# Optimization experiments

Hardware: AMD Instinct MI355X
Metric: run time of the kernel (lower is better)

The kernel has to match this reference:

```python
import jax, jax.numpy as jnp
import numpy as np

N_LAYERS = 6
N_HEADS = 16
HIDDEN = 1024
HEAD = HIDDEN // N_HEADS  # 64
FFWD = 4096
VOCAB = 32000
WIN = 512
EMBED = 128
BATCH = 4
NEG_INF = -1.0e9


def layer_norm(x, bias, scale, eps=1e-6):
    m = jnp.mean(x, axis=-1, keepdims=True)
    v = jnp.mean(jnp.square(x - m), axis=-1, keepdims=True)
    return (x - m) * jax.lax.rsqrt(v + eps) * scale + bias


def setup_inputs() -> dict:
    key = jax.random.key(0)
    ks = jax.random.split(key, 16)

    def rn(k, shape):
        return 0.1 * jax.random.normal(k, shape, jnp.float32)

    return {
        "x_input": jax.random.randint(ks[0], (BATCH, WIN), 0, VOCAB),
        "prev_inputs": jax.random.normal(ks[1], (N_LAYERS, BATCH, WIN, HIDDEN), jnp.float32),
        "W_emb_dec": rn(ks[2], (VOCAB, EMBED)),
        "W_dec_lin": rn(ks[3], (EMBED, HIDDEN)),
        "p_decoder": rn(ks[4], (HIDDEN, VOCAB)),
        "p_d_q": rn(ks[5], (N_LAYERS, HIDDEN, HIDDEN)),
        "p_d_k": rn(ks[6], (N_LAYERS, HIDDEN, HIDDEN)),
        "p_d_v": rn(ks[7], (N_LAYERS, HIDDEN, HIDDEN)),
        "p_d_c": rn(ks[8], (N_LAYERS, HIDDEN, HIDDEN)),
        "p_d_ff1": rn(ks[9], (N_LAYERS, HIDDEN, FFWD)),
        "p_d_ff2": rn(ks[10], (N_LAYERS, FFWD, HIDDEN)),
        "b_d_ff1": jnp.zeros((N_LAYERS, FFWD), jnp.float32),
        "b_d_ff2": jnp.zeros((N_LAYERS, HIDDEN), jnp.float32),
        "b_d_bias_1": jnp.zeros((N_LAYERS, HIDDEN), jnp.float32),
        "b_d_bias_2": jnp.zeros((N_LAYERS, HIDDEN), jnp.float32),
        "b_d_scale_1": jnp.ones((N_LAYERS, HIDDEN), jnp.float32),
        "b_d_scale_2": jnp.ones((N_LAYERS, HIDDEN), jnp.float32),
        "x_emb_pos_dec": rn(ks[11], (N_LAYERS, 2 * WIN, HIDDEN)),
    }


def reference(x_input, prev_inputs, W_emb_dec, W_dec_lin, p_decoder,
              p_d_q, p_d_k, p_d_v, p_d_c, p_d_ff1, p_d_ff2,
              b_d_ff1, b_d_ff2, b_d_bias_1, b_d_bias_2,
              b_d_scale_1, b_d_scale_2, x_emb_pos_dec):
    L = x_input.shape[1]
    # token embedding (scaled by 1/sqrt(hidden)) then linear to hidden
    tok = W_emb_dec[x_input] * (HIDDEN ** -0.5)        # [B, L, E]
    h0 = jnp.einsum('ble,eh->blh', tok, W_dec_lin)     # [B, L, H]

    mask_len = L + WIN
    mask = NEG_INF * (1.0 - jnp.tril(jnp.ones((mask_len, mask_len), jnp.float32)))

    def split_heads(x):
        b, t, _ = x.shape
        return x.reshape(b, t, N_HEADS, HEAD).transpose(0, 2, 1, 3)  # [B, nH, T, d]

    def layer_fn(layer_input, p):
        Wq, Wk, Wv, Wc, Wf1, Wf2, bf1, bf2, b1, s1, b2, s2, pos, prev = p
        # concat cached window with current input, add positional embedding
        x = pos[None] + jnp.concatenate([prev, layer_input], axis=1)  # [B, 2W, H]
        q = split_heads(x @ Wq) * (HEAD ** -0.5)
        k = split_heads(x @ Wk)
        v = split_heads(x @ Wv)
        scores = jnp.einsum('bhqd,bhkd->bhqk', q, k) + mask
        alphas = jax.nn.softmax(scores, axis=-1)
        o = jnp.einsum('bhqk,bhkd->bhqd', alphas, v)
        o = o.transpose(0, 2, 1, 3).reshape(x.shape)  # combine heads
        attn = o @ Wc
        # var_type == 'norm_add': residual + LN(sublayer)
        x_self = x + layer_norm(attn, b1, s1)
        ff = jnp.maximum(x_self @ Wf1 + bf1, 0.0) @ Wf2 + bf2
        y = x_self + layer_norm(ff, b2, s2)
        new = y[:, WIN:, :]  # drop the cached-window positions
        return new, new

    params = (p_d_q, p_d_k, p_d_v, p_d_c, p_d_ff1, p_d_ff2,
              b_d_ff1, b_d_ff2, b_d_bias_1, b_d_scale_1,
              b_d_bias_2, b_d_scale_2, x_emb_pos_dec, prev_inputs)
    _, dec_outputs = jax.lax.scan(layer_fn, h0, params)  # [n_layers, B, L, H]
    dec_logits = jnp.einsum('blh,hv->blv', dec_outputs[-1], p_decoder)
    return (dec_logits, dec_outputs)
```

## Files before the change

### kernel.cpp

```cpp
#include <hip/hip_runtime.h>
#include <hip/hip_bf16.h>

#define NL   6
#define NH   16
#define HID  1024
#define HD   64
#define FFW  4096
#define VOC  32000
#define WINN 512
#define EMB  128
#define NB   4
#define TT   1024

typedef __attribute__((ext_vector_type(8))) _Float16 f16x8;
typedef __attribute__((ext_vector_type(8))) short    b16x8;
typedef __attribute__((ext_vector_type(4))) float    f32x4;

__device__ __forceinline__ ushort f2b(float f) {
    __hip_bfloat16 h = __float2bfloat16(f);
    return *reinterpret_cast<ushort*>(&h);
}
__device__ __forceinline__ void split16(float f, ushort& hb, ushort& lb) {
    _Float16 h = (_Float16)f;
    _Float16 l = (_Float16)((f - (float)h) * 2048.0f);
    hb = __builtin_bit_cast(ushort, h);
    lb = __builtin_bit_cast(ushort, l);
}

__global__ __launch_bounds__(256) void embed_kernel(
    const int* __restrict__ xin, const float* __restrict__ Wemb,
    const float* __restrict__ Wlin, float* __restrict__ h0)
{
    int row = blockIdx.x;
    int tok = xin[row];
    __shared__ float tk[EMB];
    if (threadIdx.x < EMB) tk[threadIdx.x] = Wemb[tok * EMB + threadIdx.x] * 0.03125f;
    __syncthreads();
    for (int j = 0; j < 4; ++j) {
        int c = threadIdx.x + 256 * j;
        float acc = 0.f;
        for (int e = 0; e < EMB; ++e) acc += tk[e] * Wlin[e * HID + c];
        h0[(long)row * HID + c] = acc;
    }
}

__global__ __launch_bounds__(256) void build_x_kernel(
    const float* __restrict__ pos, const float* __restrict__ prev,
    const float* __restrict__ cur, float* __restrict__ x,
    ushort* __restrict__ xh, ushort* __restrict__ xl)
{
    int i4 = blockIdx.x * blockDim.x + threadIdx.x;
    if (i4 >= NB * TT * HID / 4) return;
    int h4 = i4 % (HID / 4);
    int bt = i4 / (HID / 4);
    int t = bt % TT, b = bt / TT;
    float4 p = ((const float4*)pos)[t * (HID / 4) + h4];
    float4 s;
    if (t < WINN) s = ((const float4*)prev)[(long)(b * WINN + t) * (HID / 4) + h4];
    else          s = ((const float4*)cur)[(long)(b * WINN + (t - WINN)) * (HID / 4) + h4];
    float4 r; r.x = p.x + s.x; r.y = p.y + s.y; r.z = p.z + s.z; r.w = p.w + s.w;
    ((float4*)x)[i4] = r;
    ushort4 uh, ul;
    split16(r.x, uh.x, ul.x); split16(r.y, uh.y, ul.y);
    split16(r.z, uh.z, ul.z); split16(r.w, uh.w, ul.w);
    ((ushort4*)xh)[i4] = uh;
    ((ushort4*)xl)[i4] = ul;
}

__global__ __launch_bounds__(256) void wsplit_kernel(
    const float* __restrict__ W, ushort* __restrict__ Wth, ushort* __restrict__ Wtl,
    int K, int N)
{
    __shared__ float ts[32][33];
    int n0 = blockIdx.x * 32, k0 = blockIdx.y * 32;
    int tr = threadIdx.x >> 5, tc = threadIdx.x & 31;
#pragma unroll
    for (int j = 0; j < 4; ++j)
        ts[tr + j * 8][tc] = W[(long)(k0 + tr + j * 8) * N + n0 + tc];
    __syncthreads();
#pragma unroll
    for (int j = 0; j < 4; ++j) {
        int n = tr + j * 8;
        ushort hb, lb;
        split16(ts[tc][n], hb, lb);
        long idx = (long)(n0 + n) * K + k0 + tc;
        Wth[idx] = hb;
        Wtl[idx] = lb;
    }
}

__global__ __launch_bounds__(256) void vtrans_kernel(
    const ushort* __restrict__ vh, const ushort* __restrict__ vl,
    ushort* __restrict__ vth, ushort* __restrict__ vtl, int src_stride)
{
    __shared__ ushort th[32][33], tl[32][33];
    int n0 = blockIdx.x * 32, r0 = blockIdx.y * 32;
    int tr = threadIdx.x >> 5, tc = threadIdx.x & 31;
#pragma unroll
    for (int j = 0; j < 4; ++j) {
        long g = (long)(r0 + tr + j * 8) * src_stride + n0 + tc;
        th[tr + j * 8][tc] = vh[g];
        tl[tr + j * 8][tc] = vl[g];
    }
    __syncthreads();
#pragma unroll
    for (int j = 0; j < 4; ++j) {
        long g = (long)(n0 + tr + j * 8) * (NB * TT) + r0 + tc;
        vth[g] = th[tc][tr + j * 8];
        vtl[g] = tl[tc][tr + j * 8];
    }
}

__global__ __launch_bounds__(256) void hgemm(
    const ushort* __restrict__ Ah, const ushort* __restrict__ Al,
    const ushort* __restrict__ Bh, const ushort* __restrict__ Bl,
    float* __restrict__ Cf0, float* __restrict__ Cf1,
    int M, int N, int K_stride, int Ksub,
    float scale, const float* __restrict__ bias, int relu, int amap)
{
    __shared__ ushort Ash[128 * 40];
    __shared__ ushort Asl[128 * 40];
    __shared__ ushort Bsh[64 * 40];
    __shared__ ushort Bsl[64 * 40];
    const int tid  = threadIdx.x;
    const int rb   = blockIdx.y * 128;
    const int cb   = blockIdx.x * 64;
    const int z    = blockIdx.z;
    const int k_off = z * Ksub;
    float* __restrict__ Cf = z ? Cf1 : Cf0;
    const float* bias_eff = (z == 0) ? bias : nullptr;
    const int wave = tid >> 6, lane = tid & 63;
    const int wr   = (wave >> 1) * 64;
    const int wc   = (wave & 1) * 32;
    const int lr   = lane & 15;
    const int kh   = lane >> 4;

    const int sar = tid >> 1;
    const int sak = (tid & 1) * 16;
    int gra = rb + sar;
    long marow = amap ? (long)((gra >> 9) * 1024 + 512 + (gra & 511)) : (long)gra;
    const ushort* pAh = Ah + marow * K_stride + k_off + sak;
    const ushort* pAl = Al + marow * K_stride + k_off + sak;
    const int wA0 = sar * 40 + sak, wA1 = wA0 + 8;
    const int sbr = tid >> 2;
    const int sbk = (tid & 3) * 8;
    const ushort* pBh = Bh + (long)(cb + sbr) * K_stride + k_off + sbk;
    const ushort* pBl = Bl + (long)(cb + sbr) * K_stride + k_off + sbk;
    const int wB0 = sbr * 40 + sbk;

    int aoff[4], boff[2];
#pragma unroll
    for (int m = 0; m < 4; ++m) aoff[m] = (wr + m * 16 + lr) * 40 + kh * 8;
#pragma unroll
    for (int n = 0; n < 2; ++n) boff[n] = (wc + n * 16 + lr) * 40 + kh * 8;

    f32x4 accH[4][2], accL[4][2];
#pragma unroll
    for (int m = 0; m < 4; ++m)
#pragma unroll
        for (int n = 0; n < 2; ++n) {
            accH[m][n] = (f32x4){0.f, 0.f, 0.f, 0.f};
            accL[m][n] = (f32x4){0.f, 0.f, 0.f, 0.f};
        }

    for (int k0 = 0; k0 < Ksub; k0 += 32) {
        uint4 ah0 = *(const uint4*)(pAh + k0);
        uint4 ah1 = *(const uint4*)(pAh + k0 + 8);
        uint4 al0 = *(const uint4*)(pAl + k0);
        uint4 al1 = *(const uint4*)(pAl + k0 + 8);
        uint4 bh0 = *(const uint4*)(pBh + k0);
        uint4 bl0 = *(const uint4*)(pBl + k0);
        __syncthreads();
        *(uint4*)(Ash + wA0) = ah0; *(uint4*)(Ash + wA1) = ah1;
        *(uint4*)(Asl + wA0) = al0; *(uint4*)(Asl + wA1) = al1;
        *(uint4*)(Bsh + wB0) = bh0;
        *(uint4*)(Bsl + wB0) = bl0;
        __syncthreads();
        f16x8 afh[4], afl[4], bfh[2], bfl[2];
#pragma unroll
        for (int m = 0; m < 4; ++m) {
            afh[m] = *(const f16x8*)(Ash + aoff[m]);
            afl[m] = *(const f16x8*)(Asl + aoff[m]);
        }
#pragma unroll
        for (int n = 0; n < 2; ++n) {
            bfh[n] = *(const f16x8*)(Bsh + boff[n]);
            bfl[n] = *(const f16x8*)(Bsl + boff[n]);
        }
#pragma unroll
        for (int m = 0; m < 4; ++m)
#pragma unroll
            for (int n = 0; n < 2; ++n) {
                accH[m][n] = __builtin_amdgcn_mfma_f32_16x16x32_f16(afh[m], bfh[n], accH[m][n], 0, 0, 0);
                accL[m][n] = __builtin_amdgcn_mfma_f32_16x16x32_f16(afh[m], bfl[n], accL[m][n], 0, 0, 0);
                accL[m][n] = __builtin_amdgcn_mfma_f32_16x16x32_f16(afl[m], bfh[n], accL[m][n], 0, 0, 0);
            }
    }

#pragma unroll
    for (int m = 0; m < 4; ++m) {
        int row0 = rb + wr + m * 16 + kh * 4;
#pragma unroll
        for (int n = 0; n < 2; ++n) {
            int col = cb + wc + n * 16 + lr;
            float bv = bias_eff ? bias_eff[col] : 0.f;
#pragma unroll
            for (int r = 0; r < 4; ++r) {
                float v = (accH[m][n][r] + accL[m][n][r] * (1.f / 2048.f)) * scale + bv;
                if (relu) v = fmaxf(v, 0.f);
                Cf[(long)(row0 + r) * N + col] = v;
            }
        }
    }
}

__global__ __launch_bounds__(512) void hgemm8(
    const ushort* __restrict__ Ah, const ushort* __restrict__ Al,
    const ushort* __restrict__ Bh, const ushort* __restrict__ Bl,
    ushort* __restrict__ Chh, ushort* __restrict__ Cll,
    int M, int N, int K_stride,
    float scale, const float* __restrict__ bias, int relu)
{
    __shared__ ushort Ash[128 * 40];
    __shared__ ushort Asl[128 * 40];
    __shared__ ushort Bsh[128 * 40];
    __shared__ ushort Bsl[128 * 40];
    const int tid  = threadIdx.x;
    const int rb   = blockIdx.y * 128;
    const int cb   = blockIdx.x * 128;
    const int wave = tid >> 6, lane = tid & 63;
    const int wr   = (wave >> 2) * 64;
    const int wc   = (wave & 3) * 32;
    const int lr   = lane & 15;
    const int kh   = lane >> 4;

    const int srow = tid >> 2;
    const int sk   = (tid & 3) * 8;
    const ushort* pAh = Ah + (long)(rb + srow) * K_stride + sk;
    const ushort* pAl = Al + (long)(rb + srow) * K_stride + sk;
    const ushort* pBh = Bh + (long)(cb + srow) * K_stride + sk;
    const ushort* pBl = Bl + (long)(cb + srow) * K_stride + sk;
    const int woff = srow * 40 + sk;

    int aoff[4], boff[2];
#pragma unroll
    for (int m = 0; m < 4; ++m) aoff[m] = (wr + m * 16 + lr) * 40 + kh * 8;
#pragma unroll
    for (int n = 0; n < 2; ++n) boff[n] = (wc + n * 16 + lr) * 40 + kh * 8;

    f32x4 accH[4][2], accL[4][2];
#pragma unroll
    for (int m = 0; m < 4; ++m)
#pragma unroll
        for (int n = 0; n < 2; ++n) {
            accH[m][n] = (f32x4){0.f, 0.f, 0.f, 0.f};
            accL[m][n] = (f32x4){0.f, 0.f, 0.f, 0.f};
        }

    for (int k0 = 0; k0 < K_stride; k0 += 32) {
        uint4 ah = *(const uint4*)(pAh + k0);
        uint4 al = *(const uint4*)(pAl + k0);
        uint4 bh = *(const uint4*)(pBh + k0);
        uint4 bl = *(const uint4*)(pBl + k0);
        __syncthreads();
        *(uint4*)(Ash + woff) = ah;
        *(uint4*)(Asl + woff) = al;
        *(uint4*)(Bsh + woff) = bh;
        *(uint4*)(Bsl + woff) = bl;
        __syncthreads();
        f16x8 afh[4], afl[4], bfh[2], bfl[2];
#pragma unroll
        for (int m = 0; m < 4; ++m) {
            afh[m] = *(const f16x8*)(Ash + aoff[m]);
            afl[m] = *(const f16x8*)(Asl + aoff[m]);
        }
#pragma unroll
        for (int n = 0; n < 2; ++n) {
            bfh[n] = *(const f16x8*)(Bsh + boff[n]);
            bfl[n] = *(const f16x8*)(Bsl + boff[n]);
        }
#pragma unroll
        for (int m = 0; m < 4; ++m)
#pragma unroll
            for (int n = 0; n < 2; ++n) {
                accH[m][n] = __builtin_amdgcn_mfma_f32_16x16x32_f16(afh[m], bfh[n], accH[m][n], 0, 0, 0);
                accL[m][n] = __builtin_amdgcn_mfma_f32_16x16x32_f16(afh[m], bfl[n], accL[m][n], 0, 0, 0);
                accL[m][n] = __builtin_amdgcn_mfma_f32_16x16x32_f16(afl[m], bfh[n], accL[m][n], 0, 0, 0);
            }
    }

#pragma unroll
    for (int m = 0; m < 4; ++m) {
        int row0 = rb + wr + m * 16 + kh * 4;
#pragma unroll
        for (int n = 0; n < 2; ++n) {
            int col = cb + wc + n * 16 + lr;
            float bv = bias ? bias[col] : 0.f;
#pragma unroll
            for (int r = 0; r < 4; ++r) {
                float v = (accH[m][n][r] + accL[m][n][r] * (1.f / 2048.f)) * scale + bv;
                if (relu) v = fmaxf(v, 0.f);
                long idx = (long)(row0 + r) * N + col;
                ushort hb, lb; split16(v, hb, lb);
                Chh[idx] = hb; Cll[idx] = lb;
            }
        }
    }
}

__global__ __launch_bounds__(256) void fattn_mfma(
    const float* __restrict__ qa, const float* __restrict__ qb,
    const ushort* __restrict__ kbh, const ushort* __restrict__ kbl, int kstr,
    const ushort* __restrict__ vth, const ushort* __restrict__ vtl,
    ushort* __restrict__ oh, ushort* __restrict__ ol)
{
    __shared__ __align__(16) ushort ksh[64 * 72];
    __shared__ __align__(16) ushort ksl[64 * 72];
    __shared__ __align__(16) ushort vsh[64 * 72];
    __shared__ __align__(16) ushort vsl[64 * 72];
    const int qt = blockIdx.x, h = blockIdx.y, b = blockIdx.z;
    const int tid = threadIdx.x;
    const int wave = tid >> 6, lane = tid & 63;
    const int lr = lane & 15, kg4 = lane >> 4;
    const int qbase = b * WINN + qt * 64;

    f16x8 qfh[2], qfl[2];
#pragma unroll
    for (int c = 0; c < 2; ++c) {
        long ga = (long)(qbase + wave * 16 + lr) * HID + h * HD + c * 32 + kg4 * 8;
        float4 a0 = *(const float4*)(qa + ga);
        float4 a1 = *(const float4*)(qa + ga + 4);
        float4 b0 = *(const float4*)(qb + ga);
        float4 b1 = *(const float4*)(qb + ga + 4);
        float qv[8] = {a0.x + b0.x, a0.y + b0.y, a0.z + b0.z, a0.w + b0.w,
                       a1.x + b1.x, a1.y + b1.y, a1.z + b1.z, a1.w + b1.w};
        ushort uh[8], ul[8];
#pragma unroll
        for (int j = 0; j < 8; ++j) split16(qv[j], uh[j], ul[j]);
        qfh[c] = *(const f16x8*)uh;
        qfl[c] = *(const f16x8*)ul;
    }

    f32x4 accOH[4], accOL[4];
#pragma unroll
    for (int d = 0; d < 4; ++d) {
        accOH[d] = (f32x4){0.f, 0.f, 0.f, 0.f};
        accOL[d] = (f32x4){0.f, 0.f, 0.f, 0.f};
    }
    float mrow[4], lrow[4];
#pragma unroll
    for (int r = 0; r < 4; ++r) { mrow[r] = -3.0e38f; lrow[r] = 0.f; }

    const int sr = tid >> 2;
    const int sd = (tid & 3) * 16;

    const int ktmax = 9 + qt;
    for (int kt = 0; kt < ktmax; ++kt) {
        __syncthreads();
        {
            long gk = (long)(b * TT + kt * 64 + sr) * kstr + h * HD + sd;
            uint4 h0 = *(const uint4*)(kbh + gk);
            uint4 h1 = *(const uint4*)(kbh + gk + 8);
            uint4 l0 = *(const uint4*)(kbl + gk);
            uint4 l1 = *(const uint4*)(kbl + gk + 8);
            long gv = (long)(h * HD + sr) * (NB * TT) + b * TT + kt * 64 + sd;
            uint4 vh0 = *(const uint4*)(vth + gv);
            uint4 vh1 = *(const uint4*)(vth + gv + 8);
            uint4 vl0 = *(const uint4*)(vtl + gv);
            uint4 vl1 = *(const uint4*)(vtl + gv + 8);
            *(uint4*)(ksh + sr * 72 + sd) = h0;
            *(uint4*)(ksh + sr * 72 + sd + 8) = h1;
            *(uint4*)(ksl + sr * 72 + sd) = l0;
            *(uint4*)(ksl + sr * 72 + sd + 8) = l1;
            *(uint4*)(vsh + sr * 72 + sd) = vh0;
            *(uint4*)(vsh + sr * 72 + sd + 8) = vh1;
            *(uint4*)(vsl + sr * 72 + sd) = vl0;
            *(uint4*)(vsl + sr * 72 + sd + 8) = vl1;
        }
        __syncthreads();

        f32x4 sH[4], sL[4];
#pragma unroll
        for (int n = 0; n < 4; ++n) {
            sH[n] = (f32x4){0.f, 0.f, 0.f, 0.f};
            sL[n] = (f32x4){0.f, 0.f, 0.f, 0.f};
        }
#pragma unroll
        for (int c = 0; c < 2; ++c) {
#pragma unroll
            for (int n = 0; n < 4; ++n) {
                int ad = (n * 16 + lr) * 72 + c * 32 + kg4 * 8;
                f16x8 bh = *(const f16x8*)(ksh + ad);
                f16x8 bl = *(const f16x8*)(ksl + ad);
                sH[n] = __builtin_amdgcn_mfma_f32_16x16x32_f16(qfh[c], bh, sH[n], 0, 0, 0);
                sL[n] = __builtin_amdgcn_mfma_f32_16x16x32_f16(qfh[c], bl, sL[n], 0, 0, 0);
                sL[n] = __builtin_amdgcn_mfma_f32_16x16x32_f16(qfl[c], bh, sL[n], 0, 0, 0);
            }
        }
        float S[4][4];
#pragma unroll
        for (int n = 0; n < 4; ++n)
#pragma unroll
            for (int r = 0; r < 4; ++r)
                S[n][r] = sH[n][r] + sL[n][r] * (1.f / 2048.f);

        if (kt == ktmax - 1) {
#pragma unroll
            for (int r = 0; r < 4; ++r) {
                int qi = WINN + qt * 64 + wave * 16 + kg4 * 4 + r;
#pragma unroll
                for (int n = 0; n < 4; ++n) {
                    int kg = kt * 64 + n * 16 + lr;
                    if (kg > qi) S[n][r] = -1e9f;
                }
            }
        }

#pragma unroll
        for (int r = 0; r < 4; ++r) {
            float mx = fmaxf(fmaxf(S[0][r], S[1][r]), fmaxf(S[2][r], S[3][r]));
            mx = fmaxf(mx, __shfl_xor(mx, 1));
            mx = fmaxf(mx, __shfl_xor(mx, 2));
            mx = fmaxf(mx, __shfl_xor(mx, 4));
            mx = fmaxf(mx, __shfl_xor(mx, 8));
            float mnew = fmaxf(mrow[r], mx);
            float alpha = __expf(mrow[r] - mnew);
            float rs = 0.f;
#pragma unroll
            for (int n = 0; n < 4; ++n) { S[n][r] = __expf(S[n][r] - mnew); rs += S[n][r]; }
            rs += __shfl_xor(rs, 1);
            rs += __shfl_xor(rs, 2);
            rs += __shfl_xor(rs, 4);
            rs += __shfl_xor(rs, 8);
            lrow[r] = lrow[r] * alpha + rs;
            mrow[r] = mnew;
#pragma unroll
            for (int d = 0; d < 4; ++d) { accOH[d][r] *= alpha; accOL[d][r] *= alpha; }
        }

        __syncthreads();
#pragma unroll
        for (int n = 0; n < 4; ++n)
#pragma unroll
            for (int r = 0; r < 4; ++r) {
                ushort hb, lb;
                split16(S[n][r], hb, lb);
                int ad = (wave * 16 + kg4 * 4 + r) * 72 + n * 16 + lr;
                ksh[ad] = hb;
                ksl[ad] = lb;
            }
        f16x8 pfh[2], pfl[2];
#pragma unroll
        for (int c = 0; c < 2; ++c) {
            int ad = (wave * 16 + lr) * 72 + c * 32 + kg4 * 8;
            pfh[c] = *(const f16x8*)(ksh + ad);
            pfl[c] = *(const f16x8*)(ksl + ad);
        }
#pragma unroll
        for (int c = 0; c < 2; ++c) {
#pragma unroll
            for (int d = 0; d < 4; ++d) {
                int ad = (d * 16 + lr) * 72 + c * 32 + kg4 * 8;
                f16x8 vh = *(const f16x8*)(vsh + ad);
                f16x8 vl = *(const f16x8*)(vsl + ad);
                accOH[d] = __builtin_amdgcn_mfma_f32_16x16x32_f16(pfh[c], vh, accOH[d], 0, 0, 0);
                accOL[d] = __builtin_amdgcn_mfma_f32_16x16x32_f16(pfh[c], vl, accOL[d], 0, 0, 0);
                accOL[d] = __builtin_amdgcn_mfma_f32_16x16x32_f16(pfl[c], vh, accOL[d], 0, 0, 0);
            }
        }
    }

#pragma unroll
    for (int r = 0; r < 4; ++r) {
        float inv = 1.f / lrow[r];
        long rowb = (long)(qbase + wave * 16 + kg4 * 4 + r) * HID + h * HD + lr;
#pragma unroll
        for (int d = 0; d < 4; ++d) {
            float v = (accOH[d][r] + accOL[d][r] * (1.f / 2048.f)) * inv;
            ushort hb, lb;
            split16(v, hb, lb);
            oh[rowb + d * 16] = hb;
            ol[rowb + d * 16] = lb;
        }
    }
}

__global__ __launch_bounds__(256) void transp_kernel(
    const float* __restrict__ W, ushort* __restrict__ Wt, int K, int N)
{
    __shared__ float ts[32][33];
    int n0 = blockIdx.x * 32, k0 = blockIdx.y * 32;
    int tr = threadIdx.x >> 5, tc = threadIdx.x & 31;
#pragma unroll
    for (int j = 0; j < 4; ++j)
        ts[tr + j * 8][tc] = W[(long)(k0 + tr + j * 8) * N + n0 + tc];
    __syncthreads();
#pragma unroll
    for (int j = 0; j < 4; ++j) {
        int n = tr + j * 8;
        Wt[(long)(n0 + n) * K + k0 + tc] = f2b(ts[tc][n]);
    }
}

__global__ __launch_bounds__(256) void mfma_gemm(
    const ushort* __restrict__ A, const ushort* __restrict__ Bt,
    float* __restrict__ Cf, int M, int N, int K)
{
    __shared__ ushort As[128 * 40];
    __shared__ ushort Bs[128 * 40];
    const int tid  = threadIdx.x;
    const int nbx = gridDim.x;
    const int nwg = nbx * gridDim.y;
    const int bid = blockIdx.y * nbx + blockIdx.x;
    const int cpx = nwg >> 3;
    const int swz = (bid & 7) * cpx + (bid >> 3);
    const int rb  = (swz / nbx) * 128;
    const int cb  = (swz % nbx) * 128;
    const int wave = tid >> 6, lane = tid & 63;
    const int wr   = (wave >> 1) * 64;
    const int wc   = (wave & 1) * 64;
    const int lr   = lane & 15;
    const int kh   = lane >> 4;

    const int srow = tid >> 1;
    const int kc0  = (tid & 1) * 2;
    const ushort* aptr = A + (long)(rb + srow) * K + kc0 * 8;
    const ushort* bptr = Bt + (long)(cb + srow) * K + kc0 * 8;
    const int woff0 = srow * 40 + kc0 * 8;
    const int woff1 = srow * 40 + (kc0 + 1) * 8;

    int aoff[4], boff[4];
#pragma unroll
    for (int m = 0; m < 4; ++m) aoff[m] = (wr + m * 16 + lr) * 40 + kh * 8;
#pragma unroll
    for (int n = 0; n < 4; ++n) boff[n] = (wc + n * 16 + lr) * 40 + kh * 8;

    f32x4 acc[4][4];
#pragma unroll
    for (int m = 0; m < 4; ++m)
#pragma unroll
        for (int n = 0; n < 4; ++n)
            acc[m][n] = (f32x4){0.f, 0.f, 0.f, 0.f};

    for (int k0 = 0; k0 < K; k0 += 32) {
        uint4 a0 = *(const uint4*)(aptr + k0);
        uint4 a1 = *(const uint4*)(aptr + k0 + 8);
        uint4 b0 = *(const uint4*)(bptr + k0);
        uint4 b1 = *(const uint4*)(bptr + k0 + 8);
        __syncthreads();
        *(uint4*)(As + woff0) = a0;
        *(uint4*)(As + woff1) = a1;
        *(uint4*)(Bs + woff0) = b0;
        *(uint4*)(Bs + woff1) = b1;
        __syncthreads();
        b16x8 af[4], bfr[4];
#pragma unroll
        for (int m = 0; m < 4; ++m) af[m] = *(const b16x8*)(As + aoff[m]);
#pragma unroll
        for (int n = 0; n < 4; ++n) bfr[n] = *(const b16x8*)(Bs + boff[n]);
#pragma unroll
        for (int m = 0; m < 4; ++m)
#pragma unroll
            for (int n = 0; n < 4; ++n)
                acc[m][n] = __builtin_amdgcn_mfma_f32_16x16x32_bf16(af[m], bfr[n], acc[m][n], 0, 0, 0);
    }

#pragma unroll
    for (int m = 0; m < 4; ++m) {
        int row0 = rb + wr + m * 16 + kh * 4;
#pragma unroll
        for (int n = 0; n < 4; ++n) {
            int col = cb + wc + n * 16 + lr;
#pragma unroll
            for (int r = 0; r < 4; ++r)
                Cf[(long)(row0 + r) * N + col] = acc[m][n][r];
        }
    }
}

__global__ __launch_bounds__(256) void ln_res_kernel(
    const float* __restrict__ t, const float* __restrict__ t2,
    const float* __restrict__ res, float* __restrict__ out,
    ushort* __restrict__ outh, ushort* __restrict__ outl, ushort* __restrict__ outb,
    const float* __restrict__ bias, const float* __restrict__ scale, int res_map)
{
    int r = blockIdx.x;
    int tid = threadIdx.x;
    long rr = res_map ? (long)((r >> 9) * 1024 + 512 + (r & 511)) : (long)r;
    float4 v = ((const float4*)(t + (long)r * HID))[tid];
    if (t2) {
        float4 w = ((const float4*)(t2 + (long)r * HID))[tid];
        v.x += w.x; v.y += w.y; v.z += w.z; v.w += w.w;
    }
    __shared__ float red[4];
    float s = v.x + v.y + v.z + v.w;
    for (int off = 32; off > 0; off >>= 1) s += __shfl_xor(s, off);
    if ((tid & 63) == 0) red[tid >> 6] = s;
    __syncthreads();
    float mean = (red[0] + red[1] + red[2] + red[3]) * (1.f / HID);
    __syncthreads();
    float dx = v.x - mean, dy = v.y - mean, dz = v.z - mean, dw = v.w - mean;
    float qs = dx * dx + dy * dy + dz * dz + dw * dw;
    for (int off = 32; off > 0; off >>= 1) qs += __shfl_xor(qs, off);
    if ((tid & 63) == 0) red[tid >> 6] = qs;
    __syncthreads();
    float var = (red[0] + red[1] + red[2] + red[3]) * (1.f / HID);
    float rs = rsqrtf(var + 1e-6f);
    float4 rv = ((const float4*)(res + rr * HID))[tid];
    float4 sc4 = ((const float4*)scale)[tid];
    float4 b4  = ((const float4*)bias)[tid];
    float4 o4;
    o4.x = rv.x + dx * rs * sc4.x + b4.x;
    o4.y = rv.y + dy * rs * sc4.y + b4.y;
    o4.z = rv.z + dz * rs * sc4.z + b4.z;
    o4.w = rv.w + dw * rs * sc4.w + b4.w;
    ((float4*)(out + (long)r * HID))[tid] = o4;
    if (outh) {
        ushort4 uh, ul;
        split16(o4.x, uh.x, ul.x); split16(o4.y, uh.y, ul.y);
        split16(o4.z, uh.z, ul.z); split16(o4.w, uh.w, ul.w);
        ((ushort4*)(outh + (long)r * HID))[tid] = uh;
        ((ushort4*)(outl + (long)r * HID))[tid] = ul;
    }
    if (outb) {
        ushort4 u; u.x = f2b(o4.x); u.y = f2b(o4.y); u.z = f2b(o4.z); u.w = f2b(o4.w);
        ((ushort4*)(outb + (long)r * HID))[tid] = u;
    }
}

extern "C" void kernel_launch(void* const* d_in, const int* in_sizes, int n_in,
                              void* d_out, int out_size, void* d_ws, size_t ws_size,
                              hipStream_t stream)
{
    const int*   x_input = (const int*)  d_in[0];
    const float* prev    = (const float*)d_in[1];
    const float* Wemb    = (const float*)d_in[2];
    const float* Wlin    = (const float*)d_in[3];
    const float* pdec    = (const float*)d_in[4];
    const float* pq      = (const float*)d_in[5];
    const float* pk      = (const float*)d_in[6];
    const float* pv      = (const float*)d_in[7];
    const float* pc      = (const float*)d_in[8];
    const float* pf1     = (const float*)d_in[9];
    const float* pf2     = (const float*)d_in[10];
    const float* bf1     = (const float*)d_in[11];
    const float* bf2     = (const float*)d_in[12];
    const float* b1      = (const float*)d_in[13];
    const float* b2      = (const float*)d_in[14];
    const float* s1      = (const float*)d_in[15];
    const float* s2      = (const float*)d_in[16];
    const float* pos     = (const float*)d_in[17];

    float* outp   = (float*)d_out;
    float* logits = outp;
    float* dec    = outp + (long)2048 * VOC;

    char* base = (char*)d_ws;
    float*  x_f   = (float*) (base + 0);
    ushort* x_hi  = (ushort*)(base + 16777216);
    ushort* x_lo  = (ushort*)(base + 25165824);
    ushort* kv_hi = (ushort*)(base + 33554432);
    ushort* kv_lo = (ushort*)(base + 50331648);
    ushort* vt_hi = (ushort*)(base + 67108864);
    ushort* vt_lo = (ushort*)(base + 75497472);
    ushort* o_hi  = (ushort*)(base + 83886080);
    ushort* o_lo  = (ushort*)(base + 88080384);
    float*  t0a   = (float*) (base + 92274688);
    float*  h0    = t0a;
    float*  qa    = t0a;
    float*  t0b   = (float*) (base + 100663296);
    float*  qb    = t0b;
    float*  xs    = (float*) (base + 109051904);
    ushort* xs_hi = (ushort*)(base + 117440512);
    ushort* xs_lo = (ushort*)(base + 121634816);
    ushort* wq_hi = (ushort*)(base + 125829120);
    ushort* wq_lo = (ushort*)(base + 127926272);
    ushort* wkv_hi= (ushort*)(base + 130023424);
    ushort* wkv_lo= (ushort*)(base + 134217728);
    ushort* wc_hi = (ushort*)(base + 138412032);
    ushort* wc_lo = (ushort*)(base + 140509184);
    ushort* wf1_hi= (ushort*)(base + 142606336);
    ushort* wf1_lo= (ushort*)(base + 150994944);
    ushort* wf2_hi= (ushort*)(base + 159383552);
    ushort* wf2_lo= (ushort*)(base + 167772160);
    ushort* ff1_hi= (ushort*)(base + 33554432);
    ushort* ff1_lo= (ushort*)(base + 50331648);
    ushort* decb  = (ushort*)(base + 83886080);
    ushort* wdect = (ushort*)(base + 0);

    embed_kernel<<<NB * WINN, 256, 0, stream>>>(x_input, Wemb, Wlin, h0);

    for (int l = 0; l < NL; ++l) {
        const float* cur = (l == 0) ? h0 : (dec + (long)(l - 1) * 2097152);
        build_x_kernel<<<(NB * TT * HID / 4) / 256, 256, 0, stream>>>(
            pos + (long)l * TT * HID, prev + (long)l * NB * WINN * HID, cur,
            x_f, x_hi, x_lo);

        wsplit_kernel<<<dim3(32, 32), 256, 0, stream>>>(pq + (long)l * HID * HID, wq_hi, wq_lo, HID, HID);
        wsplit_kernel<<<dim3(32, 32), 256, 0, stream>>>(pk + (long)l * HID * HID, wkv_hi, wkv_lo, HID, HID);
        wsplit_kernel<<<dim3(32, 32), 256, 0, stream>>>(pv + (long)l * HID * HID,
                                                        wkv_hi + (size_t)1024 * 1024,
                                                        wkv_lo + (size_t)1024 * 1024, HID, HID);
        wsplit_kernel<<<dim3(32, 32), 256, 0, stream>>>(pc + (long)l * HID * HID, wc_hi, wc_lo, HID, HID);
        wsplit_kernel<<<dim3(FFW / 32, HID / 32), 256, 0, stream>>>(
            pf1 + (long)l * HID * FFW, wf1_hi, wf1_lo, HID, FFW);
        wsplit_kernel<<<dim3(HID / 32, FFW / 32), 256, 0, stream>>>(
            pf2 + (long)l * FFW * HID, wf2_hi, wf2_lo, FFW, HID);

        hgemm8<<<dim3(2048 / 128, (NB * TT) / 128), 512, 0, stream>>>(
            x_hi, x_lo, wkv_hi, wkv_lo, kv_hi, kv_lo,
            NB * TT, 2048, HID, 1.f, nullptr, 0);
        hgemm<<<dim3(HID / 64, (NB * WINN) / 128, 2), 256, 0, stream>>>(
            x_hi, x_lo, wq_hi, wq_lo, qa, qb,
            NB * WINN, HID, HID, 512, 0.125f, nullptr, 0, 1);
        vtrans_kernel<<<dim3(HID / 32, (NB * TT) / 32), 256, 0, stream>>>(
            kv_hi + 1024, kv_lo + 1024, vt_hi, vt_lo, 2048);

        fattn_mfma<<<dim3(WINN / 64, NH, NB), 256, 0, stream>>>(
            qa, qb, kv_hi, kv_lo, 2048, vt_hi, vt_lo, o_hi, o_lo);

        hgemm<<<dim3(HID / 64, (NB * WINN) / 128, 2), 256, 0, stream>>>(
            o_hi, o_lo, wc_hi, wc_lo, t0a, t0b,
            NB * WINN, HID, HID, 512, 1.f, nullptr, 0, 0);
        ln_res_kernel<<<NB * WINN, 256, 0, stream>>>(
            t0a, t0b, x_f, xs, xs_hi, xs_lo, nullptr,
            b1 + l * HID, s1 + l * HID, 1);

        hgemm8<<<dim3(FFW / 128, (NB * WINN) / 128), 512, 0, stream>>>(
            xs_hi, xs_lo, wf1_hi, wf1_lo, ff1_hi, ff1_lo,
            NB * WINN, FFW, HID, 1.f, bf1 + l * FFW, 1);
        hgemm<<<dim3(HID / 64, (NB * WINN) / 128, 2), 256, 0, stream>>>(
            ff1_hi, ff1_lo, wf2_hi, wf2_lo, t0a, t0b,
            NB * WINN, HID, FFW, 2048, 1.f, bf2 + l * HID, 0, 0);
        ln_res_kernel<<<NB * WINN, 256, 0, stream>>>(
            t0a, t0b, xs, dec + (long)l * 2097152, nullptr, nullptr,
            (l == NL - 1) ? decb : nullptr, b2 + l * HID, s2 + l * HID, 0);
    }

    transp_kernel<<<dim3(VOC / 32, HID / 32), 256, 0, stream>>>(pdec, wdect, HID, VOC);
    mfma_gemm<<<dim3(VOC / 128, (NB * WINN) / 128), 256, 0, stream>>>(
        decb, wdect, logits, NB * WINN, VOC, HID);
}
```

Measured before the change: 2.610 ms.

## Load GEMM tiles directly into LDS via global_load_lds and reorder tile swizzle

Replaces the register-staged global-to-shared copies in the three MFMA GEMM kernels with direct global-to-LDS loads (global_load_lds, 16 bytes per lane). This drops the VGPR round trip and the explicit shared-memory stores. Because that instruction writes lanes contiguously, the LDS row stride goes from a padded 40 to an unpadded 32 elements, which may add bank conflicts on the fragment reads. The loads also lose overlap with the previous iteration's compute, since they now issue after the barrier. The bf16 GEMM's tile swizzle is also changed to walk row tiles first, for better reuse of B in cache.

```diff
diff --git a/kernel.cpp b/kernel.cpp
--- a/kernel.cpp
+++ b/kernel.cpp
@@ -25,6 +25,11 @@
     _Float16 l = (_Float16)((f - (float)h) * 2048.0f);
     hb = __builtin_bit_cast(ushort, h);
     lb = __builtin_bit_cast(ushort, l);
+}
+__device__ __forceinline__ void gload16(const void* g, void* l) {
+    __builtin_amdgcn_global_load_lds(
+        (const __attribute__((address_space(1))) unsigned int*)g,
+        (__attribute__((address_space(3))) unsigned int*)l, 16, 0, 0);
 }
 
 __global__ __launch_bounds__(256) void embed_kernel(
@@ -118,10 +123,10 @@
     int M, int N, int K_stride, int Ksub,
     float scale, const float* __restrict__ bias, int relu, int amap)
 {
-    __shared__ ushort Ash[128 * 40];
-    __shared__ ushort Asl[128 * 40];
-    __shared__ ushort Bsh[64 * 40];
-    __shared__ ushort Bsl[64 * 40];
+    __shared__ __align__(16) ushort Ash[128 * 32];
+    __shared__ __align__(16) ushort Asl[128 * 32];
+    __shared__ __align__(16) ushort Bsh[64 * 32];
+    __shared__ __align__(16) ushort Bsl[64 * 32];
     const int tid  = threadIdx.x;
     const int rb   = blockIdx.y * 128;
     const int cb   = blockIdx.x * 64;
@@ -135,24 +140,30 @@
     const int lr   = lane & 15;
     const int kh   = lane >> 4;
 
-    const int sar = tid >> 1;
-    const int sak = (tid & 1) * 16;
-    int gra = rb + sar;
-    long marow = amap ? (long)((gra >> 9) * 1024 + 512 + (gra & 511)) : (long)gra;
-    const ushort* pAh = Ah + marow * K_stride + k_off + sak;
-    const ushort* pAl = Al + marow * K_stride + k_off + sak;
-    const int wA0 = sar * 40 + sak, wA1 = wA0 + 8;
-    const int sbr = tid >> 2;
-    const int sbk = (tid & 3) * 8;
-    const ushort* pBh = Bh + (long)(cb + sbr) * K_stride + k_off + sbk;
-    const ushort* pBl = Bl + (long)(cb + sbr) * K_stride + k_off + sbk;
-    const int wB0 = sbr * 40 + sbk;
+    const int lrow = lane >> 2;
+    const int lkc  = (lane & 3) * 8;
+    int ga0 = rb + wave * 32 + lrow;
+    int ga1 = ga0 + 16;
+    long ma0 = amap ? (long)((ga0 >> 9) * 1024 + 512 + (ga0 & 511)) : (long)ga0;
+    long ma1 = amap ? (long)((ga1 >> 9) * 1024 + 512 + (ga1 & 511)) : (long)ga1;
+    const ushort* gAh0 = Ah + ma0 * K_stride + k_off + lkc;
+    const ushort* gAh1 = Ah + ma1 * K_stride + k_off + lkc;
+    const ushort* gAl0 = Al + ma0 * K_stride + k_off + lkc;
+    const ushort* gAl1 = Al + ma1 * K_stride + k_off + lkc;
+    const ushort* gBh0 = Bh + (long)(cb + wave * 16 + lrow) * K_stride + k_off + lkc;
+    const ushort* gBl0 = Bl + (long)(cb + wave * 16 + lrow) * K_stride + k_off + lkc;
+    ushort* lAh0 = Ash + wave * 1024;
+    ushort* lAh1 = Ash + wave * 1024 + 512;
+    ushort* lAl0 = Asl + wave * 1024;
+    ushort* lAl1 = Asl + wave * 1024 + 512;
+    ushort* lBh0 = Bsh + wave * 512;
+    ushort* lBl0 = Bsl + wave * 512;
 
     int aoff[4], boff[2];
 #pragma unroll
-    for (int m = 0; m < 4; ++m) aoff[m] = (wr + m * 16 + lr) * 40 + kh * 8;
-#pragma unroll
-    for (int n = 0; n < 2; ++n) boff[n] = (wc + n * 16 + lr) * 40 + kh * 8;
+    for (int m = 0; m < 4; ++m) aoff[m] = (wr + m * 16 + lr) * 32 + kh * 8;
+#pragma unroll
+    for (int n = 0; n < 2; ++n) boff[n] = (wc + n * 16 + lr) * 32 + kh * 8;
 
     f32x4 accH[4][2], accL[4][2];
 #pragma unroll
@@ -164,17 +175,13 @@
         }
 
     for (int k0 = 0; k0 < Ksub; k0 += 32) {
-        uint4 ah0 = *(const uint4*)(pAh + k0);
-        uint4 ah1 = *(const uint4*)(pAh + k0 + 8);
-        uint4 al0 = *(const uint4*)(pAl + k0);
-        uint4 al1 = *(const uint4*)(pAl + k0 + 8);
-        uint4 bh0 = *(const uint4*)(pBh + k0);
-        uint4 bl0 = *(const uint4*)(pBl + k0);
-        __syncthreads();
-        *(uint4*)(Ash + wA0) = ah0; *(uint4*)(Ash + wA1) = ah1;
-        *(uint4*)(Asl + wA0) = al0; *(uint4*)(Asl + wA1) = al1;
-        *(uint4*)(Bsh + wB0) = bh0;
-        *(uint4*)(Bsl + wB0) = bl0;
+        __syncthreads();
+        gload16(gAh0 + k0, lAh0);
+        gload16(gAh1 + k0, lAh1);
+        gload16(gAl0 + k0, lAl0);
+        gload16(gAl1 + k0, lAl1);
+        gload16(gBh0 + k0, lBh0);
+        gload16(gBl0 + k0, lBl0);
         __syncthreads();
         f16x8 afh[4], afl[4], bfh[2], bfl[2];
 #pragma unroll
@@ -221,10 +228,10 @@
     int M, int N, int K_stride,
     float scale, const float* __restrict__ bias, int relu)
 {
-    __shared__ ushort Ash[128 * 40];
-    __shared__ ushort Asl[128 * 40];
-    __shared__ ushort Bsh[128 * 40];
-    __shared__ ushort Bsl[128 * 40];
+    __shared__ __align__(16) ushort Ash[128 * 32];
+    __shared__ __align__(16) ushort Asl[128 * 32];
+    __shared__ __align__(16) ushort Bsh[128 * 32];
+    __shared__ __align__(16) ushort Bsl[128 * 32];
     const int tid  = threadIdx.x;
     const int rb   = blockIdx.y * 128;
     const int cb   = blockIdx.x * 128;
@@ -234,19 +241,22 @@
     const int lr   = lane & 15;
     const int kh   = lane >> 4;
 
-    const int srow = tid >> 2;
-    const int sk   = (tid & 3) * 8;
-    const ushort* pAh = Ah + (long)(rb + srow) * K_stride + sk;
-    const ushort* pAl = Al + (long)(rb + srow) * K_stride + sk;
-    const ushort* pBh = Bh + (long)(cb + srow) * K_stride + sk;
-    const ushort* pBl = Bl + (long)(cb + srow) * K_stride + sk;
-    const int woff = srow * 40 + sk;
+    const int lrow = lane >> 2;
+    const int lkc  = (lane & 3) * 8;
+    const ushort* gA_h = Ah + (long)(rb + wave * 16 + lrow) * K_stride + lkc;
+    const ushort* gA_l = Al + (long)(rb + wave * 16 + lrow) * K_stride + lkc;
+    const ushort* gB_h = Bh + (long)(cb + wave * 16 + lrow) * K_stride + lkc;
+    const ushort* gB_l = Bl + (long)(cb + wave * 16 + lrow) * K_stride + lkc;
+    ushort* lA_h = Ash + wave * 512;
+    ushort* lA_l = Asl + wave * 512;
+    ushort* lB_h = Bsh + wave * 512;
+    ushort* lB_l = Bsl + wave * 512;
 
     int aoff[4], boff[2];
 #pragma unroll
-    for (int m = 0; m < 4; ++m) aoff[m] = (wr + m * 16 + lr) * 40 + kh * 8;
-#pragma unroll
-    for (int n = 0; n < 2; ++n) boff[n] = (wc + n * 16 + lr) * 40 + kh * 8;
+    for (int m = 0; m < 4; ++m) aoff[m] = (wr + m * 16 + lr) * 32 + kh * 8;
+#pragma unroll
+    for (int n = 0; n < 2; ++n) boff[n] = (wc + n * 16 + lr) * 32 + kh * 8;
 
     f32x4 accH[4][2], accL[4][2];
 #pragma unroll
@@ -258,15 +268,11 @@
         }
 
     for (int k0 = 0; k0 < K_stride; k0 += 32) {
-        uint4 ah = *(const uint4*)(pAh + k0);
-        uint4 al = *(const uint4*)(pAl + k0);
-        uint4 bh = *(const uint4*)(pBh + k0);
-        uint4 bl = *(const uint4*)(pBl + k0);
-        __syncthreads();
-        *(uint4*)(Ash + woff) = ah;
-        *(uint4*)(Asl + woff) = al;
-        *(uint4*)(Bsh + woff) = bh;
-        *(uint4*)(Bsl + woff) = bl;
+        __syncthreads();
+        gload16(gA_h + k0, lA_h);
+        gload16(gA_l + k0, lA_l);
+        gload16(gB_h + k0, lB_h);
+        gload16(gB_l + k0, lB_l);
         __syncthreads();
         f16x8 afh[4], afl[4], bfh[2], bfl[2];
 #pragma unroll
@@ -506,34 +512,39 @@
     const ushort* __restrict__ A, const ushort* __restrict__ Bt,
     float* __restrict__ Cf, int M, int N, int K)
 {
-    __shared__ ushort As[128 * 40];
-    __shared__ ushort Bs[128 * 40];
+    __shared__ __align__(16) ushort As[128 * 32];
+    __shared__ __align__(16) ushort Bs[128 * 32];
     const int tid  = threadIdx.x;
-    const int nbx = gridDim.x;
-    const int nwg = nbx * gridDim.y;
-    const int bid = blockIdx.y * nbx + blockIdx.x;
-    const int cpx = nwg >> 3;
-    const int swz = (bid & 7) * cpx + (bid >> 3);
-    const int rb  = (swz / nbx) * 128;
-    const int cb  = (swz % nbx) * 128;
+    const int ntm  = M >> 7;
+    const int nbx  = gridDim.x;
+    const int nwg  = nbx * gridDim.y;
+    const int bid  = blockIdx.y * nbx + blockIdx.x;
+    const int cpx  = nwg >> 3;
+    const int swz  = (bid & 7) * cpx + (bid >> 3);
+    const int rb   = (swz % ntm) * 128;
+    const int cb   = (swz / ntm) * 128;
     const int wave = tid >> 6, lane = tid & 63;
     const int wr   = (wave >> 1) * 64;
     const int wc   = (wave & 1) * 64;
     const int lr   = lane & 15;
     const int kh   = lane >> 4;
 
-    const int srow = tid >> 1;
-    const int kc0  = (tid & 1) * 2;
-    const ushort* aptr = A + (long)(rb + srow) * K + kc0 * 8;
-    const ushort* bptr = Bt + (long)(cb + srow) * K + kc0 * 8;
-    const int woff0 = srow * 40 + kc0 * 8;
-    const int woff1 = srow * 40 + (kc0 + 1) * 8;
+    const int lrow = lane >> 2;
+    const int lkc  = (lane & 3) * 8;
+    const ushort* gA0 = A + (long)(rb + wave * 32 + lrow) * K + lkc;
+    const ushort* gA1 = A + (long)(rb + wave * 32 + 16 + lrow) * K + lkc;
+    const ushort* gB0 = Bt + (long)(cb + wave * 32 + lrow) * K + lkc;
+    const ushort* gB1 = Bt + (long)(cb + wave * 32 + 16 + lrow) * K + lkc;
+    ushort* lA0 = As + wave * 1024;
+    ushort* lA1 = As + wave * 1024 + 512;
+    ushort* lB0 = Bs + wave * 1024;
+    ushort* lB1 = Bs + wave * 1024 + 512;
 
     int aoff[4], boff[4];
 #pragma unroll
-    for (int m = 0; m < 4; ++m) aoff[m] = (wr + m * 16 + lr) * 40 + kh * 8;
-#pragma unroll
-    for (int n = 0; n < 4; ++n) boff[n] = (wc + n * 16 + lr) * 40 + kh * 8;
+    for (int m = 0; m < 4; ++m) aoff[m] = (wr + m * 16 + lr) * 32 + kh * 8;
+#pragma unroll
+    for (int n = 0; n < 4; ++n) boff[n] = (wc + n * 16 + lr) * 32 + kh * 8;
 
     f32x4 acc[4][4];
 #pragma unroll
@@ -543,15 +554,11 @@
             acc[m][n] = (f32x4){0.f, 0.f, 0.f, 0.f};
 
     for (int k0 = 0; k0 < K; k0 += 32) {
-        uint4 a0 = *(const uint4*)(aptr + k0);
-        uint4 a1 = *(const uint4*)(aptr + k0 + 8);
-        uint4 b0 = *(const uint4*)(bptr + k0);
-        uint4 b1 = *(const uint4*)(bptr + k0 + 8);
-        __syncthreads();
-        *(uint4*)(As + woff0) = a0;
-        *(uint4*)(As + woff1) = a1;
-        *(uint4*)(Bs + woff0) = b0;
-        *(uint4*)(Bs + woff1) = b1;
+        __syncthreads();
+        gload16(gA0 + k0, lA0);
+        gload16(gA1 + k0, lA1);
+        gload16(gB0 + k0, lB0);
+        gload16(gB1 + k0, lB1);
         __syncthreads();
         b16x8 af[4], bfr[4];
 #pragma unroll
```

New measurement: 2.548 ms. -2.4%, faster.
